# Performance work log

Measured on AMD Instinct MI355X. Metric: run time of the kernel, lower is better.

The kernel has to match this reference:

```python
import jax, jax.numpy as jnp
import numpy as np

B, C, H, W = 32, 3, 128, 128
NMIX = 10  # 10 logistic mixture components -> 100 param channels for RGB


def setup_inputs() -> dict:
    key = jax.random.key(0)
    k1, k2 = jax.random.split(key)
    samples = jax.random.uniform(k1, (B, C, H, W), dtype=jnp.float32)  # pixel values in [0,1]
    params = jax.random.normal(k2, (B, 10 * NMIX, H, W), dtype=jnp.float32)  # PixelCNN output params
    return {"samples": samples, "params": params}


def _discretized_mix_logistic_log_prob(x, l):
    # x: [B,H,W,3] in [-1,1]; l: [B,H,W,100]
    logit_probs = l[..., :NMIX]                                   # [B,H,W,NMIX]
    rest = l[..., NMIX:].reshape(l.shape[0], l.shape[1], l.shape[2], 3, 3 * NMIX)
    means = rest[..., :NMIX]                                      # [B,H,W,3,NMIX]
    log_scales = jnp.maximum(rest[..., NMIX:2 * NMIX], -7.0)
    coeffs = jnp.tanh(rest[..., 2 * NMIX:3 * NMIX])

    x0 = x[..., 0:1]  # [B,H,W,1]
    x1 = x[..., 1:2]
    m1 = means[..., 0, :]
    m2 = means[..., 1, :] + coeffs[..., 0, :] * x0
    m3 = means[..., 2, :] + coeffs[..., 1, :] * x0 + coeffs[..., 2, :] * x1
    means_c = jnp.stack([m1, m2, m3], axis=3)                     # [B,H,W,3,NMIX]

    xb = x[..., None]                                             # [B,H,W,3,1]
    centered = xb - means_c
    inv_stdv = jnp.exp(-log_scales)
    plus_in = inv_stdv * (centered + 1.0 / 255.0)
    min_in = inv_stdv * (centered - 1.0 / 255.0)
    cdf_plus = jax.nn.sigmoid(plus_in)
    cdf_min = jax.nn.sigmoid(min_in)
    log_cdf_plus = plus_in - jax.nn.softplus(plus_in)             # log CDF at left edge bin (x = -1)
    log_one_minus_cdf_min = -jax.nn.softplus(min_in)              # log(1-CDF) at right edge bin (x = 1)
    cdf_delta = cdf_plus - cdf_min
    mid_in = inv_stdv * centered
    log_pdf_mid = mid_in - log_scales - 2.0 * jax.nn.softplus(mid_in)

    inner = jnp.where(cdf_delta > 1e-5,
                      jnp.log(jnp.maximum(cdf_delta, 1e-12)),
                      log_pdf_mid - np.float32(np.log(127.5)))
    log_probs_ch = jnp.where(xb < -0.999, log_cdf_plus,
                             jnp.where(xb > 0.999, log_one_minus_cdf_min, inner))
    # sum over channels, mixture weights, logsumexp over mixtures
    log_probs = log_probs_ch.sum(axis=3) + jax.nn.log_softmax(logit_probs, axis=-1)
    return jax.scipy.special.logsumexp(log_probs, axis=-1).sum()


def reference(samples, params):
    # _PixelCNNDistribution.log_prob: rescale samples to [-1,1], evaluate
    # discretized mixture-of-logistics log-likelihood (= -discretized_mix_logistic_loss).
    x = jnp.transpose(samples * 2.0 - 1.0, (0, 2, 3, 1))  # NCHW -> NHWC
    l = jnp.transpose(params, (0, 2, 3, 1))
    return _discretized_mix_logistic_log_prob(x, l)
```

## Files before the change

### kernel.cpp

```cpp
#include <hip/hip_runtime.h>
#include <math.h>

#define HW 16384
#define HW4 4096
#define NMIX 10
#define NPIX (32 * HW)
#define NQUAD (NPIX / 4)

__device__ __forceinline__ float fexp(float x) { return __expf(x); }
__device__ __forceinline__ float flog(float x) { return __logf(x); }
__device__ __forceinline__ float frcp(float x) { return __builtin_amdgcn_rcpf(x); }

__device__ __forceinline__ float ftanh(float y) {
    float t = fexp(-2.0f * fabsf(y));
    float r = (1.0f - t) * frcp(1.0f + t);
    return (y >= 0.0f) ? r : -r;
}

__device__ __forceinline__ float channel_logprob(float x, float mean, float ls) {
    const float INV255 = 0.00392156862745098f;
    const float LOG127_5 = 4.852030263919617f;
    float inv = fexp(-ls);
    float centered = x - mean;
    float plus_in = inv * (centered + INV255);
    float min_in  = inv * (centered - INV255);
    float mid_in  = inv * centered;

    float tp = fexp(-fabsf(plus_in));
    float rp = frcp(1.0f + tp);
    float sp_plus  = fmaxf(plus_in, 0.0f) + flog(1.0f + tp);
    float sig_plus = (plus_in >= 0.0f) ? rp : tp * rp;

    float tm = fexp(-fabsf(min_in));
    float rm = frcp(1.0f + tm);
    float sp_min  = fmaxf(min_in, 0.0f) + flog(1.0f + tm);
    float sig_min = (min_in >= 0.0f) ? rm : tm * rm;

    float tmid = fexp(-fabsf(mid_in));
    float sp_mid = fmaxf(mid_in, 0.0f) + flog(1.0f + tmid);

    float log_cdf_plus    = plus_in - sp_plus;
    float log_om_cdf_min  = -sp_min;
    float cdf_delta       = sig_plus - sig_min;
    float log_pdf_mid     = mid_in - ls - 2.0f * sp_mid;

    float inner = (cdf_delta > 1e-5f) ? flog(fmaxf(cdf_delta, 1e-12f))
                                      : (log_pdf_mid - LOG127_5);
    return (x < -0.999f) ? log_cdf_plus
         : ((x > 0.999f) ? log_om_cdf_min : inner);
}

__global__ __launch_bounds__(256) void pixelcnn_kernel(
    const float4* __restrict__ samples, const float4* __restrict__ params,
    float* __restrict__ out)
{
    int q  = blockIdx.x * blockDim.x + threadIdx.x;
    int b  = q >> 12;
    int hw = q & (HW4 - 1);

    const float4* sp = samples + (size_t)b * 3   * HW4 + hw;
    const float4* pp = params  + (size_t)b * 100 * HW4 + hw;

    float4 s0 = sp[0];
    float4 s1 = sp[HW4];
    float4 s2 = sp[2 * HW4];
    const float* fs0 = (const float*)&s0;
    const float* fs1 = (const float*)&s1;
    const float* fs2 = (const float*)&s2;

    float x0[4], x1[4], x2[4], mr[4], sr[4], ml[4], sl[4];
    #pragma unroll
    for (int j = 0; j < 4; ++j) {
        x0[j] = 2.0f * fs0[j] - 1.0f;
        x1[j] = 2.0f * fs1[j] - 1.0f;
        x2[j] = 2.0f * fs2[j] - 1.0f;
        mr[j] = -3.4e38f; sr[j] = 0.0f;
        ml[j] = -3.4e38f; sl[j] = 0.0f;
    }

    #pragma unroll 1
    for (int k = 0; k < NMIX; ++k) {
        float4 vlogit = pp[(size_t)(k)      * HW4];
        float4 vmean0 = pp[(size_t)(10 + k) * HW4];
        float4 vlsc0  = pp[(size_t)(20 + k) * HW4];
        float4 vcw0   = pp[(size_t)(30 + k) * HW4];
        float4 vmean1 = pp[(size_t)(40 + k) * HW4];
        float4 vlsc1  = pp[(size_t)(50 + k) * HW4];
        float4 vcw1   = pp[(size_t)(60 + k) * HW4];
        float4 vmean2 = pp[(size_t)(70 + k) * HW4];
        float4 vlsc2  = pp[(size_t)(80 + k) * HW4];
        float4 vcw2   = pp[(size_t)(90 + k) * HW4];
        const float* logit = (const float*)&vlogit;
        const float* mean0 = (const float*)&vmean0;
        const float* lsc0  = (const float*)&vlsc0;
        const float* cw0   = (const float*)&vcw0;
        const float* mean1 = (const float*)&vmean1;
        const float* lsc1  = (const float*)&vlsc1;
        const float* cw1   = (const float*)&vcw1;
        const float* mean2 = (const float*)&vmean2;
        const float* lsc2  = (const float*)&vlsc2;
        const float* cw2   = (const float*)&vcw2;

        #pragma unroll
        for (int j = 0; j < 4; ++j) {
            float ls0 = fmaxf(lsc0[j], -7.0f);
            float ls1 = fmaxf(lsc1[j], -7.0f);
            float ls2 = fmaxf(lsc2[j], -7.0f);
            float c0 = ftanh(cw0[j]);
            float c1 = ftanh(cw1[j]);
            float c2 = ftanh(cw2[j]);

            float m1 = mean0[j];
            float m2 = mean1[j] + c0 * x0[j];
            float m3 = mean2[j] + c1 * x0[j] + c2 * x1[j];

            float lp = channel_logprob(x0[j], m1, ls0)
                     + channel_logprob(x1[j], m2, ls1)
                     + channel_logprob(x2[j], m3, ls2);
            float raw = lp + logit[j];

            float nm = fmaxf(mr[j], raw);
            sr[j] = sr[j] * fexp(mr[j] - nm) + fexp(raw - nm);
            mr[j] = nm;
            float nl = fmaxf(ml[j], logit[j]);
            sl[j] = sl[j] * fexp(ml[j] - nl) + fexp(logit[j] - nl);
            ml[j] = nl;
        }
    }

    float val = 0.0f;
    #pragma unroll
    for (int j = 0; j < 4; ++j)
        val += (mr[j] + flog(sr[j])) - (ml[j] + flog(sl[j]));

    #pragma unroll
    for (int off = 32; off > 0; off >>= 1)
        val += __shfl_down(val, off, 64);

    __shared__ float wsum[4];
    int lane = threadIdx.x & 63;
    int wid  = threadIdx.x >> 6;
    if (lane == 0) wsum[wid] = val;
    __syncthreads();
    if (threadIdx.x == 0) {
        float bsum = (wsum[0] + wsum[1]) + (wsum[2] + wsum[3]);
        atomicAdd(out, bsum);
    }
}

extern "C" void kernel_launch(void* const* d_in, const int* in_sizes, int n_in,
                              void* d_out, int out_size, void* d_ws, size_t ws_size,
                              hipStream_t stream) {
    const float4* samples = (const float4*)d_in[0];
    const float4* params  = (const float4*)d_in[1];
    float* out = (float*)d_out;

    hipMemsetAsync(out, 0, sizeof(float), stream);
    pixelcnn_kernel<<<NQUAD / 256, 256, 0, stream>>>(samples, params, out);
}
```

Measured before the change: 295.8 us.

## Skip edge-bin softplus per wave, prefetch next mixture, use 2 pixels per thread

Each thread now handles 2 pixels through float2 loads instead of 4, which doubles the thread count for better latency hiding. The next mixture's 10 parameter loads are software-prefetched into registers. A wave ballot skips the edge-bin softplus logs when no lane has a sample near ±1. The online logsumexp update is also rewritten to use a single exp per update. The trade-off is more registers for the prefetch buffers, and the wave-uniform branch only saves work when no lane in the wave hits an edge value.

```diff
diff --git a/kernel.cpp b/kernel.cpp
--- a/kernel.cpp
+++ b/kernel.cpp
@@ -2,10 +2,11 @@
 #include <math.h>
 
 #define HW 16384
-#define HW4 4096
+#define HW2 8192
 #define NMIX 10
 #define NPIX (32 * HW)
-#define NQUAD (NPIX / 4)
+#define NTHREADS (NPIX / 2)
+#define NBLOCKS (NTHREADS / 256)
 
 __device__ __forceinline__ float fexp(float x) { return __expf(x); }
 __device__ __forceinline__ float flog(float x) { return __logf(x); }
@@ -17,7 +18,8 @@
     return (y >= 0.0f) ? r : -r;
 }
 
-__device__ __forceinline__ float channel_logprob(float x, float mean, float ls) {
+__device__ __forceinline__ float channel_logprob(float x, float mean, float ls,
+                                                 bool waveEdge) {
     const float INV255 = 0.00392156862745098f;
     const float LOG127_5 = 4.852030263919617f;
     float inv = fexp(-ls);
@@ -28,81 +30,91 @@
 
     float tp = fexp(-fabsf(plus_in));
     float rp = frcp(1.0f + tp);
-    float sp_plus  = fmaxf(plus_in, 0.0f) + flog(1.0f + tp);
     float sig_plus = (plus_in >= 0.0f) ? rp : tp * rp;
 
     float tm = fexp(-fabsf(min_in));
     float rm = frcp(1.0f + tm);
-    float sp_min  = fmaxf(min_in, 0.0f) + flog(1.0f + tm);
     float sig_min = (min_in >= 0.0f) ? rm : tm * rm;
+
+    float cdf_delta = sig_plus - sig_min;
 
     float tmid = fexp(-fabsf(mid_in));
     float sp_mid = fmaxf(mid_in, 0.0f) + flog(1.0f + tmid);
+    float log_pdf_mid = mid_in - ls - 2.0f * sp_mid;
 
-    float log_cdf_plus    = plus_in - sp_plus;
-    float log_om_cdf_min  = -sp_min;
-    float cdf_delta       = sig_plus - sig_min;
-    float log_pdf_mid     = mid_in - ls - 2.0f * sp_mid;
-
-    float inner = (cdf_delta > 1e-5f) ? flog(fmaxf(cdf_delta, 1e-12f))
-                                      : (log_pdf_mid - LOG127_5);
-    return (x < -0.999f) ? log_cdf_plus
-         : ((x > 0.999f) ? log_om_cdf_min : inner);
+    float r = (cdf_delta > 1e-5f) ? flog(fmaxf(cdf_delta, 1e-12f))
+                                  : (log_pdf_mid - LOG127_5);
+    if (waveEdge) {
+        float sp_plus = fmaxf(plus_in, 0.0f) + flog(1.0f + tp);
+        float sp_min  = fmaxf(min_in, 0.0f) + flog(1.0f + tm);
+        float log_cdf_plus   = plus_in - sp_plus;
+        float log_om_cdf_min = -sp_min;
+        r = (x < -0.999f) ? log_cdf_plus
+          : ((x > 0.999f) ? log_om_cdf_min : r);
+    }
+    return r;
 }
 
-__global__ __launch_bounds__(256) void pixelcnn_kernel(
-    const float4* __restrict__ samples, const float4* __restrict__ params,
+__device__ __forceinline__ void lse_update(float& m, float& s, float v) {
+    float d = v - m;
+    float e = fexp(-fabsf(d));
+    bool grow = (d > 0.0f);
+    s = grow ? (s * e + 1.0f) : (s + e);
+    m = grow ? v : m;
+}
+
+__global__ __launch_bounds__(256, 4) void pixelcnn_kernel(
+    const float2* __restrict__ samples, const float2* __restrict__ params,
     float* __restrict__ out)
 {
     int q  = blockIdx.x * blockDim.x + threadIdx.x;
-    int b  = q >> 12;
-    int hw = q & (HW4 - 1);
+    int b  = q >> 13;
+    int hw = q & (HW2 - 1);
 
-    const float4* sp = samples + (size_t)b * 3   * HW4 + hw;
-    const float4* pp = params  + (size_t)b * 100 * HW4 + hw;
+    const float2* sp = samples + (size_t)b * 3   * HW2 + hw;
+    const float2* pp = params  + (size_t)b * 100 * HW2 + hw;
 
-    float4 s0 = sp[0];
-    float4 s1 = sp[HW4];
-    float4 s2 = sp[2 * HW4];
-    const float* fs0 = (const float*)&s0;
-    const float* fs1 = (const float*)&s1;
-    const float* fs2 = (const float*)&s2;
+    float2 s0 = sp[0];
+    float2 s1 = sp[HW2];
+    float2 s2 = sp[2 * HW2];
 
-    float x0[4], x1[4], x2[4], mr[4], sr[4], ml[4], sl[4];
+    float x0[2] = {2.0f * s0.x - 1.0f, 2.0f * s0.y - 1.0f};
+    float x1[2] = {2.0f * s1.x - 1.0f, 2.0f * s1.y - 1.0f};
+    float x2[2] = {2.0f * s2.x - 1.0f, 2.0f * s2.y - 1.0f};
+
+    bool edge = false;
     #pragma unroll
-    for (int j = 0; j < 4; ++j) {
-        x0[j] = 2.0f * fs0[j] - 1.0f;
-        x1[j] = 2.0f * fs1[j] - 1.0f;
-        x2[j] = 2.0f * fs2[j] - 1.0f;
-        mr[j] = -3.4e38f; sr[j] = 0.0f;
-        ml[j] = -3.4e38f; sl[j] = 0.0f;
-    }
+    for (int j = 0; j < 2; ++j)
+        edge |= (fabsf(x0[j]) > 0.999f) | (fabsf(x1[j]) > 0.999f)
+              | (fabsf(x2[j]) > 0.999f);
+    bool waveEdge = (__ballot(edge) != 0ULL);
+
+    float mr[2] = {-3.4e38f, -3.4e38f}, sr[2] = {0.0f, 0.0f};
+    float ml[2] = {-3.4e38f, -3.4e38f}, sl[2] = {0.0f, 0.0f};
+
+    float2 cur[10], nxt[10];
+    #pragma unroll
+    for (int f = 0; f < 10; ++f) cur[f] = pp[(size_t)(10 * f) * HW2];
 
     #pragma unroll 1
     for (int k = 0; k < NMIX; ++k) {
-        float4 vlogit = pp[(size_t)(k)      * HW4];
-        float4 vmean0 = pp[(size_t)(10 + k) * HW4];
-        float4 vlsc0  = pp[(size_t)(20 + k) * HW4];
-        float4 vcw0   = pp[(size_t)(30 + k) * HW4];
-        float4 vmean1 = pp[(size_t)(40 + k) * HW4];
-        float4 vlsc1  = pp[(size_t)(50 + k) * HW4];
-        float4 vcw1   = pp[(size_t)(60 + k) * HW4];
-        float4 vmean2 = pp[(size_t)(70 + k) * HW4];
-        float4 vlsc2  = pp[(size_t)(80 + k) * HW4];
-        float4 vcw2   = pp[(size_t)(90 + k) * HW4];
-        const float* logit = (const float*)&vlogit;
-        const float* mean0 = (const float*)&vmean0;
-        const float* lsc0  = (const float*)&vlsc0;
-        const float* cw0   = (const float*)&vcw0;
-        const float* mean1 = (const float*)&vmean1;
-        const float* lsc1  = (const float*)&vlsc1;
-        const float* cw1   = (const float*)&vcw1;
-        const float* mean2 = (const float*)&vmean2;
-        const float* lsc2  = (const float*)&vlsc2;
-        const float* cw2   = (const float*)&vcw2;
+        int kn = (k < NMIX - 1) ? k + 1 : k;
+        #pragma unroll
+        for (int f = 0; f < 10; ++f) nxt[f] = pp[(size_t)(10 * f + kn) * HW2];
+
+        const float* logit = (const float*)&cur[0];
+        const float* mean0 = (const float*)&cur[1];
+        const float* lsc0  = (const float*)&cur[2];
+        const float* cw0   = (const float*)&cur[3];
+        const float* mean1 = (const float*)&cur[4];
+        const float* lsc1  = (const float*)&cur[5];
+        const float* cw1   = (const float*)&cur[6];
+        const float* mean2 = (const float*)&cur[7];
+        const float* lsc2  = (const float*)&cur[8];
+        const float* cw2   = (const float*)&cur[9];
 
         #pragma unroll
-        for (int j = 0; j < 4; ++j) {
+        for (int j = 0; j < 2; ++j) {
             float ls0 = fmaxf(lsc0[j], -7.0f);
             float ls1 = fmaxf(lsc1[j], -7.0f);
             float ls2 = fmaxf(lsc2[j], -7.0f);
@@ -114,23 +126,21 @@
             float m2 = mean1[j] + c0 * x0[j];
             float m3 = mean2[j] + c1 * x0[j] + c2 * x1[j];
 
-            float lp = channel_logprob(x0[j], m1, ls0)
-                     + channel_logprob(x1[j], m2, ls1)
-                     + channel_logprob(x2[j], m3, ls2);
-            float raw = lp + logit[j];
+            float lp = channel_logprob(x0[j], m1, ls0, waveEdge)
+                     + channel_logprob(x1[j], m2, ls1, waveEdge)
+                     + channel_logprob(x2[j], m3, ls2, waveEdge);
 
-            float nm = fmaxf(mr[j], raw);
-            sr[j] = sr[j] * fexp(mr[j] - nm) + fexp(raw - nm);
-            mr[j] = nm;
-            float nl = fmaxf(ml[j], logit[j]);
-            sl[j] = sl[j] * fexp(ml[j] - nl) + fexp(logit[j] - nl);
-            ml[j] = nl;
+            lse_update(mr[j], sr[j], lp + logit[j]);
+            lse_update(ml[j], sl[j], logit[j]);
         }
+
+        #pragma unroll
+        for (int f = 0; f < 10; ++f) cur[f] = nxt[f];
     }
 
     float val = 0.0f;
     #pragma unroll
-    for (int j = 0; j < 4; ++j)
+    for (int j = 0; j < 2; ++j)
         val += (mr[j] + flog(sr[j])) - (ml[j] + flog(sl[j]));
 
     #pragma unroll
@@ -151,10 +161,10 @@
 extern "C" void kernel_launch(void* const* d_in, const int* in_sizes, int n_in,
                               void* d_out, int out_size, void* d_ws, size_t ws_size,
                               hipStream_t stream) {
-    const float4* samples = (const float4*)d_in[0];
-    const float4* params  = (const float4*)d_in[1];
+    const float2* samples = (const float2*)d_in[0];
+    const float2* params  = (const float2*)d_in[1];
     float* out = (float*)d_out;
 
     hipMemsetAsync(out, 0, sizeof(float), stream);
-    pixelcnn_kernel<<<NQUAD / 256, 256, 0, stream>>>(samples, params, out);
+    pixelcnn_kernel<<<NBLOCKS, 256, 0, stream>>>(samples, params, out);
 }
```

Measured after the change: 295.2 us. About the same (-0.2%).
